# Optimization experiments

Measured on AMD Instinct MI355X. Metric: run time of the kernel, lower is better.

Reference implementation:

```python
import jax, jax.numpy as jnp
import numpy as np

EARTH_RADIUS = 6371.0
TAU = 75.0
EPS = 1e-9


def setup_inputs() -> dict:
    key = jax.random.key(0)
    k1, k2, k3 = jax.random.split(key, 3)
    B, C = 512, 32768
    pred_logits = jax.random.normal(k1, (B, C), dtype=jnp.float32)
    # lat in [-90, 90], lon in [-180, 180]
    u_true = jax.random.uniform(k2, (B, 2), dtype=jnp.float32)
    latlon = u_true * jnp.array([180.0, 360.0], jnp.float32) - jnp.array([90.0, 180.0], jnp.float32)
    u_geo = jax.random.uniform(k3, (C, 2), dtype=jnp.float32)
    geocell_coords = u_geo * jnp.array([180.0, 360.0], jnp.float32) - jnp.array([90.0, 180.0], jnp.float32)
    return {"pred_logits": pred_logits, "latlon": latlon, "geocell_coords": geocell_coords}


def _haversine_matrix(latlon, geocell_coords):
    # latlon: [B,2] degrees, geocell_coords: [C,2] degrees -> [B,C] km
    t = jnp.deg2rad(latlon)          # [B,2]
    g = jnp.deg2rad(geocell_coords)  # [C,2]
    lat1 = t[:, 0:1]                 # [B,1]
    lon1 = t[:, 1:2]
    lat2 = g[None, :, 0]             # [1,C]
    lon2 = g[None, :, 1]
    dlat = lat2 - lat1               # [B,C]
    dlon = lon2 - lon1
    a = jnp.sin(dlat * 0.5) ** 2 + jnp.cos(lat1) * jnp.cos(lat2) * jnp.sin(dlon * 0.5) ** 2
    return 2.0 * EARTH_RADIUS * jnp.arcsin(jnp.sqrt(a))


def reference(pred_logits, latlon, geocell_coords):
    dist = _haversine_matrix(latlon, geocell_coords)          # [B,C]
    target = jnp.exp(-dist / TAU)                              # [B,C]
    target = target / jnp.sum(target, axis=1, keepdims=True)
    pred_probs = jax.nn.softmax(pred_logits, axis=1)
    loss = jnp.mean(jnp.sum(-target * jnp.log(pred_probs + EPS), axis=1))
    return loss
```

## Files before the change

kernel.cpp:

```cpp
#include <hip/hip_runtime.h>
#include <math.h>

#define PI_F 3.14159265358979323846f
#define LOG2E_F 1.4426950408889634f

#define A0c -192.49617f
#define A1c  25.995080f
#define A2c  -9.1008444f
#define A3c   2.2953158f

constexpr int CHUNK = 4096;
constexpr int ROWS  = 4;
constexpr int TPB   = 512;

__global__ void precompute(const float* __restrict__ geo,
                           const float* __restrict__ latlon,
                           float4* __restrict__ tab, float4* __restrict__ rowtab,
                           int C, int B) {
    int i = blockIdx.x * blockDim.x + threadIdx.x;
    if (i < C) {
        float lat = geo[2 * i + 0] * (PI_F / 180.0f);
        float lon = geo[2 * i + 1] * (PI_F / 180.0f);
        float sla, cla, slo, clo;
        __sincosf(lat, &sla, &cla);
        __sincosf(lon, &slo, &clo);
        tab[i] = make_float4(cla * clo, cla * slo, sla, 0.0f);
    }
    if (i < B) {
        float lat = latlon[2 * i + 0] * (PI_F / 180.0f);
        float lon = latlon[2 * i + 1] * (PI_F / 180.0f);
        float sla, cla, slo, clo;
        __sincosf(lat, &sla, &cla);
        __sincosf(lon, &slo, &clo);
        rowtab[i] = make_float4(cla * clo, cla * slo, sla, 0.0f);
    }
}

__device__ __forceinline__ void pair_accum(float l, float4 g,
                                           float vx, float vy, float vz,
                                           float& Z, float& S0, float& S1) {
    float dot = fmaf(g.x, vx, fmaf(g.y, vy, g.z * vz));
    float s = __builtin_amdgcn_sqrtf(fmaxf(fmaf(dot, -1.0f, 1.0f), 0.0f));
    float P = fmaf(fmaf(fmaf(A3c, dot, A2c), dot, A1c), dot, A0c);
    float w = exp2f(s * P);
    float el = exp2f(l * LOG2E_F);
    Z += el;
    S0 += w;
    S1 = fmaf(w, l, S1);
}

__global__ __launch_bounds__(TPB) void loss2d(
    const float* __restrict__ logits, const float4* __restrict__ tab,
    const float4* __restrict__ rowtab, float4* __restrict__ part, int C, int B) {
    const int chunk = blockIdx.x;
    const int rowbase = blockIdx.y * ROWS;
    const int t = threadIdx.x;

    float vx[ROWS], vy[ROWS], vz[ROWS];
#pragma unroll
    for (int r = 0; r < ROWS; r++) {
        float4 v = rowtab[rowbase + r];
        vx[r] = v.x; vy[r] = v.y; vz[r] = v.z;
    }
    float Z[ROWS], S0[ROWS], S1[ROWS];
#pragma unroll
    for (int r = 0; r < ROWS; r++) { Z[r] = 0.0f; S0[r] = 0.0f; S1[r] = 0.0f; }

    const int c4base = (chunk * CHUNK) >> 2;
#pragma unroll
    for (int it = 0; it < CHUNK / (TPB * 4); it++) {
        const int c4 = c4base + it * TPB + t;
        const int c = c4 << 2;
        float4 g0 = tab[c + 0], g1 = tab[c + 1], g2 = tab[c + 2], g3 = tab[c + 3];
#pragma unroll
        for (int r = 0; r < ROWS; r++) {
            float4 l4 = ((const float4*)(logits + (size_t)(rowbase + r) * C))[c4];
            pair_accum(l4.x, g0, vx[r], vy[r], vz[r], Z[r], S0[r], S1[r]);
            pair_accum(l4.y, g1, vx[r], vy[r], vz[r], Z[r], S0[r], S1[r]);
            pair_accum(l4.z, g2, vx[r], vy[r], vz[r], Z[r], S0[r], S1[r]);
            pair_accum(l4.w, g3, vx[r], vy[r], vz[r], Z[r], S0[r], S1[r]);
        }
    }

#pragma unroll
    for (int r = 0; r < ROWS; r++) {
#pragma unroll
        for (int off = 32; off > 0; off >>= 1) {
            Z[r] += __shfl_down(Z[r], off);
            S0[r] += __shfl_down(S0[r], off);
            S1[r] += __shfl_down(S1[r], off);
        }
    }
    __shared__ float red[TPB / 64][3 * ROWS];
    const int wave = t >> 6, lane = t & 63;
    if (lane == 0) {
#pragma unroll
        for (int r = 0; r < ROWS; r++) {
            red[wave][3 * r + 0] = Z[r];
            red[wave][3 * r + 1] = S0[r];
            red[wave][3 * r + 2] = S1[r];
        }
    }
    __syncthreads();
    if (t < 3 * ROWS) {
        float s = 0.0f;
#pragma unroll
        for (int w = 0; w < TPB / 64; w++) s += red[w][t];
        red[0][t] = s;
    }
    __syncthreads();
    if (t < ROWS) {
        part[(size_t)chunk * B + rowbase + t] =
            make_float4(red[0][3 * t + 0], red[0][3 * t + 1], red[0][3 * t + 2], 0.0f);
    }
}

__global__ __launch_bounds__(512) void finalize(const float4* __restrict__ part,
                                                float* __restrict__ out,
                                                int B, int nchunk, float inv_B) {
    float total = 0.0f;
    for (int r = threadIdx.x; r < B; r += blockDim.x) {
        float Z = 0.0f, S0 = 0.0f, S1 = 0.0f;
        for (int ch = 0; ch < nchunk; ch++) {
            float4 p = part[(size_t)ch * B + r];
            Z += p.x; S0 += p.y; S1 += p.z;
        }
        total += logf(Z) - S1 / S0;
    }
    for (int off = 32; off > 0; off >>= 1) total += __shfl_down(total, off);
    __shared__ float s[8];
    const int wave = threadIdx.x >> 6;
    if ((threadIdx.x & 63) == 0) s[wave] = total;
    __syncthreads();
    if (threadIdx.x == 0) {
        float tot = 0.0f;
        for (int w = 0; w < (int)(blockDim.x >> 6); w++) tot += s[w];
        out[0] = tot * inv_B;
    }
}

extern "C" void kernel_launch(void* const* d_in, const int* in_sizes, int n_in,
                              void* d_out, int out_size, void* d_ws, size_t ws_size,
                              hipStream_t stream) {
    const float* logits = (const float*)d_in[0];
    const float* latlon = (const float*)d_in[1];
    const float* geo    = (const float*)d_in[2];
    float* out = (float*)d_out;

    const int B = in_sizes[1] / 2;
    const int C = in_sizes[2] / 2;
    const int nchunk = C / CHUNK;

    float4* tab    = (float4*)d_ws;
    float4* rowtab = tab + C;
    float4* part   = rowtab + B;

    int mx = (C > B) ? C : B;
    precompute<<<(mx + 255) / 256, 256, 0, stream>>>(geo, latlon, tab, rowtab, C, B);
    dim3 grid(nchunk, B / ROWS);
    loss2d<<<grid, TPB, 0, stream>>>(logits, tab, rowtab, part, C, B);
    finalize<<<1, 512, 0, stream>>>(part, out, B, nchunk, 1.0f / (float)B);
}
```

Before: 105.4 us.

## Fuse finalize into main kernel via atomic accumulation and last-block reduction

```diff
diff --git a/kernel.cpp b/kernel.cpp
--- a/kernel.cpp
+++ b/kernel.cpp
@@ -16,6 +16,7 @@
 __global__ void precompute(const float* __restrict__ geo,
                            const float* __restrict__ latlon,
                            float4* __restrict__ tab, float4* __restrict__ rowtab,
+                           float* __restrict__ acc, int* __restrict__ counter,
                            int C, int B) {
     int i = blockIdx.x * blockDim.x + threadIdx.x;
     if (i < C) {
@@ -34,6 +35,8 @@
         __sincosf(lon, &slo, &clo);
         rowtab[i] = make_float4(cla * clo, cla * slo, sla, 0.0f);
     }
+    if (i < 3 * B) acc[i] = 0.0f;
+    if (i == 0) *counter = 0;
 }
 
 __device__ __forceinline__ void pair_accum(float l, float4 g,
@@ -51,7 +54,9 @@
 
 __global__ __launch_bounds__(TPB) void loss2d(
     const float* __restrict__ logits, const float4* __restrict__ tab,
-    const float4* __restrict__ rowtab, float4* __restrict__ part, int C, int B) {
+    const float4* __restrict__ rowtab, float* __restrict__ acc,
+    int* __restrict__ counter, float* __restrict__ out,
+    int C, int B, int nblocks, float inv_B) {
     const int chunk = blockIdx.x;
     const int rowbase = blockIdx.y * ROWS;
     const int t = threadIdx.x;
@@ -106,35 +111,40 @@
         float s = 0.0f;
 #pragma unroll
         for (int w = 0; w < TPB / 64; w++) s += red[w][t];
-        red[0][t] = s;
+        const int r = t / 3, cmp = t - 3 * r;
+        atomicAdd(&acc[3 * (rowbase + r) + cmp], s);
+    }
+    __threadfence();
+    __syncthreads();
+
+    __shared__ int slast;
+    if (t == 0) {
+        int old = __hip_atomic_fetch_add(counter, 1, __ATOMIC_ACQ_REL,
+                                         __HIP_MEMORY_SCOPE_AGENT);
+        slast = (old == nblocks - 1) ? 1 : 0;
     }
     __syncthreads();
-    if (t < ROWS) {
-        part[(size_t)chunk * B + rowbase + t] =
-            make_float4(red[0][3 * t + 0], red[0][3 * t + 1], red[0][3 * t + 2], 0.0f);
-    }
-}
+    if (!slast) return;
 
-__global__ __launch_bounds__(512) void finalize(const float4* __restrict__ part,
-                                                float* __restrict__ out,
-                                                int B, int nchunk, float inv_B) {
+    __threadfence();
     float total = 0.0f;
-    for (int r = threadIdx.x; r < B; r += blockDim.x) {
-        float Z = 0.0f, S0 = 0.0f, S1 = 0.0f;
-        for (int ch = 0; ch < nchunk; ch++) {
-            float4 p = part[(size_t)ch * B + r];
-            Z += p.x; S0 += p.y; S1 += p.z;
-        }
-        total += logf(Z) - S1 / S0;
+    for (int r = t; r < B; r += TPB) {
+        float Zr  = __hip_atomic_load(&acc[3 * r + 0], __ATOMIC_RELAXED,
+                                      __HIP_MEMORY_SCOPE_AGENT);
+        float S0r = __hip_atomic_load(&acc[3 * r + 1], __ATOMIC_RELAXED,
+                                      __HIP_MEMORY_SCOPE_AGENT);
+        float S1r = __hip_atomic_load(&acc[3 * r + 2], __ATOMIC_RELAXED,
+                                      __HIP_MEMORY_SCOPE_AGENT);
+        total += logf(Zr) - S1r / S0r;
     }
     for (int off = 32; off > 0; off >>= 1) total += __shfl_down(total, off);
-    __shared__ float s[8];
-    const int wave = threadIdx.x >> 6;
-    if ((threadIdx.x & 63) == 0) s[wave] = total;
+    __shared__ float sred[TPB / 64];
+    if (lane == 0) sred[wave] = total;
     __syncthreads();
-    if (threadIdx.x == 0) {
+    if (t == 0) {
         float tot = 0.0f;
-        for (int w = 0; w < (int)(blockDim.x >> 6); w++) tot += s[w];
+#pragma unroll
+        for (int w = 0; w < TPB / 64; w++) tot += sred[w];
         out[0] = tot * inv_B;
     }
 }
@@ -153,11 +163,13 @@
 
     float4* tab    = (float4*)d_ws;
     float4* rowtab = tab + C;
-    float4* part   = rowtab + B;
+    float*  acc    = (float*)(rowtab + B);
+    int*    counter = (int*)(acc + 3 * B);
 
     int mx = (C > B) ? C : B;
-    precompute<<<(mx + 255) / 256, 256, 0, stream>>>(geo, latlon, tab, rowtab, C, B);
+    precompute<<<(mx + 255) / 256, 256, 0, stream>>>(geo, latlon, tab, rowtab,
+                                                     acc, counter, C, B);
     dim3 grid(nchunk, B / ROWS);
-    loss2d<<<grid, TPB, 0, stream>>>(logits, tab, rowtab, part, C, B);
-    finalize<<<1, 512, 0, stream>>>(part, out, B, nchunk, 1.0f / (float)B);
+    loss2d<<<grid, TPB, 0, stream>>>(logits, tab, rowtab, acc, counter, out,
+                                     C, B, nchunk * (B / ROWS), 1.0f / (float)B);
 }
```

New measurement: 295.8 us. 181% more time.
